# Optimization experiments

Measured on AMD Instinct MI355X. Metric: run time of the kernel, lower is better.

The kernel has to match this reference:

```python
import jax, jax.numpy as jnp
import numpy as np

N = 50000
E = 800000
IN_CH = 256
HEADS = 4
OUT_CH = 32
NEG_SLOPE = 0.2
EPS = 1e-16


def setup_inputs() -> dict:
    key = jax.random.key(0)
    k1, k2, k3, k4 = jax.random.split(key, 4)
    x = jax.random.normal(k1, (N, IN_CH), dtype=jnp.float32)
    edge_index = jax.random.randint(k2, (2, E), 0, N, dtype=jnp.int32)
    # xavier-ish scaling for stability
    weight = jax.random.normal(k3, (HEADS, IN_CH, OUT_CH), dtype=jnp.float32) * (1.0 / np.sqrt(IN_CH))
    att = jax.random.normal(k4, (HEADS, 2 * OUT_CH), dtype=jnp.float32) * (1.0 / np.sqrt(2 * OUT_CH))
    bias = jnp.zeros((HEADS * OUT_CH,), dtype=jnp.float32)
    return {"x": x, "edge_index": edge_index, "weight": weight, "att": att, "bias": bias}


def reference(x, edge_index, weight, att, bias):
    n = x.shape[0]
    H, C = weight.shape[0], weight.shape[2]
    src, dst = edge_index[0], edge_index[1]
    # node features -> per-head projected features [N,H,C]
    h = jnp.einsum('nf,hfc->nhc', x, weight)
    # per-node attention logits (equivalent to concat([h_src,h_dst]) . att)
    a_src = jnp.einsum('nhc,hc->nh', h, att[:, :C])  # [N,H]
    a_dst = jnp.einsum('nhc,hc->nh', h, att[:, C:])  # [N,H]
    alpha = a_src[src] + a_dst[dst]                  # [E,H]
    alpha = jnp.where(alpha > 0, alpha, NEG_SLOPE * alpha)  # LeakyReLU(0.2)
    # segment softmax over incoming edges of each dst node
    alpha_max = jnp.full((n, H), -1e9, dtype=alpha.dtype).at[dst].max(alpha)
    alpha_exp = jnp.exp(alpha - alpha_max[dst])
    sum_exp = jax.ops.segment_sum(alpha_exp, dst, num_segments=n)  # [N,H]
    a = alpha_exp / (sum_exp[dst] + EPS)             # [E,H]
    # weighted scatter-add aggregation
    msg = h[src] * a[:, :, None]                     # [E,H,C]
    out = jax.ops.segment_sum(msg, dst, num_segments=n)  # [N,H,C]
    out = out.reshape(n, H * C) + bias[None, :]
    return out
```

## Files before the change

### kernel.cpp

```cpp
#include <hip/hip_runtime.h>
#include <hip/hip_bf16.h>

#define NEG_SLOPE 0.2f
#define EPSF 1e-16f

typedef __attribute__((ext_vector_type(8))) short short8;
typedef __attribute__((ext_vector_type(4))) float floatx4;

__device__ __forceinline__ float bf2f(unsigned short u) {
  union { unsigned int i; float f; } v; v.i = ((unsigned int)u) << 16; return v.f;
}
__device__ __forceinline__ unsigned short f2bf(float f) {
  union { float f; unsigned int i; } v; v.f = f;
  unsigned int r = v.i + 0x7fffu + ((v.i >> 16) & 1u);
  return (unsigned short)(r >> 16);
}

__global__ __launch_bounds__(256) void prep_k(const unsigned short* __restrict__ xw,
                                              const void* __restrict__ w,
                                              const void* __restrict__ att,
                                              const void* __restrict__ bias,
                                              int* __restrict__ flag,
                                              int* __restrict__ cursor,
                                              int* __restrict__ ovf_cnt,
                                              unsigned short* __restrict__ bpack,
                                              unsigned short* __restrict__ wpack,
                                              float* __restrict__ bias_f,
                                              int n, int zb) {
  int b = blockIdx.x;
  if (b < zb) {
    int i = b * 256 + threadIdx.x;
    if (i < n) cursor[i] = 0;
    if (i == 0) *ovf_cnt = 0;
    return;
  }
  __shared__ int cnt;
  if (threadIdx.x == 0) cnt = 0;
  __syncthreads();
  int local = 0;
  for (int k2 = 0; k2 < 16; k2++) {
    unsigned short u = xw[(threadIdx.x * 16 + k2) << 1];
    int ex = (u >> 7) & 0xFF;
    if (ex >= 0x90 || ex <= 0x40) local++;
  }
  atomicAdd(&cnt, local);
  __syncthreads();
  int f32 = (cnt > 256) ? 1 : 0;
  int pb = b - zb;
  if (pb == 0 && threadIdx.x == 0) *flag = f32;
  if (pb < 128) {
    int i = pb * 256 + threadIdx.x;
    int j = i & 7, lane = (i >> 3) & 63, nt = (i >> 9) & 7, kb = i >> 12;
    int f = (kb << 5) + ((lane >> 4) << 3) + j;
    int col = (nt << 4) + (lane & 15);
    int src = ((col >> 5) << 13) + (f << 5) + (col & 31);
    float v = f32 ? ((const float*)w)[src] : bf2f(((const unsigned short*)w)[src]);
    bpack[i] = f2bf(v);
  } else if (pb < 144) {
    int i = (pb - 128) * 256 + threadIdx.x;
    int j = i & 7, lane = (i >> 3) & 63, kb = i >> 9;
    int quad = lane >> 4, m16 = lane & 15;
    int f = (kb << 5) + (quad << 3) + j;
    float v = 0.f;
    if (m16 < 8) {
      int hd = m16 & 3;
      int db = (m16 >= 4) ? 32 : 0;
      int wbase = (hd << 13) + (f << 5);
      int abase = (hd << 6) + db;
      float acc = 0.f;
      for (int c = 0; c < 32; c++) {
        float wv = f32 ? ((const float*)w)[wbase + c] : bf2f(((const unsigned short*)w)[wbase + c]);
        float av = f32 ? ((const float*)att)[abase + c] : bf2f(((const unsigned short*)att)[abase + c]);
        acc = fmaf(wv, av, acc);
      }
      v = acc;
    }
    wpack[i] = f2bf(v);
  } else {
    int i = threadIdx.x;
    if (i < 128) bias_f[i] = f32 ? ((const float*)bias)[i] : bf2f(((const unsigned short*)bias)[i]);
  }
}

__global__ __launch_bounds__(256) void gemmfill_k(const void* __restrict__ xv,
                                                  const int* __restrict__ flag,
                                                  const unsigned short* __restrict__ bpack,
                                                  const unsigned short* __restrict__ wpack,
                                                  unsigned short* __restrict__ h,
                                                  float* __restrict__ a_srcp,
                                                  float* __restrict__ a_dstp,
                                                  const int* __restrict__ ei,
                                                  int* __restrict__ cursor,
                                                  unsigned short* __restrict__ ed,
                                                  int2* __restrict__ ovf,
                                                  int* __restrict__ ovf_cnt,
                                                  int n, int e, int gb, int fb) {
  int b = blockIdx.x;
  if (b < gb) {
    int t = threadIdx.x;
    int wave = t >> 6, l = t & 63;
    int quad = l >> 4, m16 = l & 15;
    long n0 = (long)b * 128 + wave * 32;
    int isf32 = *flag;

    floatx4 acc[2][8];
    floatx4 acca[2];
#pragma unroll
    for (int mt = 0; mt < 2; mt++) {
      acca[mt] = (floatx4){0.f, 0.f, 0.f, 0.f};
#pragma unroll
      for (int nt = 0; nt < 8; nt++) acc[mt][nt] = (floatx4){0.f, 0.f, 0.f, 0.f};
    }

    for (int kb = 0; kb < 8; kb++) {
      short8 afr[2];
#pragma unroll
      for (int mt = 0; mt < 2; mt++) {
        long row = n0 + mt * 16 + m16;
        if (row >= n) row = n - 1;
        if (isf32) {
          const float* xp = (const float*)xv + (row << 8) + (kb << 5) + (quad << 3);
          float4 u0 = *(const float4*)xp;
          float4 u1 = *(const float4*)(xp + 4);
          short8 a;
          a[0] = (short)f2bf(u0.x); a[1] = (short)f2bf(u0.y);
          a[2] = (short)f2bf(u0.z); a[3] = (short)f2bf(u0.w);
          a[4] = (short)f2bf(u1.x); a[5] = (short)f2bf(u1.y);
          a[6] = (short)f2bf(u1.z); a[7] = (short)f2bf(u1.w);
          afr[mt] = a;
        } else {
          afr[mt] = *(const short8*)((const unsigned short*)xv + (row << 8) + (kb << 5) + (quad << 3));
        }
      }
      short8 wfr = *(const short8*)(wpack + (((kb << 6) + l) << 3));
      acca[0] = __builtin_amdgcn_mfma_f32_16x16x32_bf16(afr[0], wfr, acca[0], 0, 0, 0);
      acca[1] = __builtin_amdgcn_mfma_f32_16x16x32_bf16(afr[1], wfr, acca[1], 0, 0, 0);
#pragma unroll
      for (int nt = 0; nt < 8; nt++) {
        short8 bfr = *(const short8*)(bpack + (((kb << 3) + nt) << 9) + (l << 3));
        acc[0][nt] = __builtin_amdgcn_mfma_f32_16x16x32_bf16(afr[0], bfr, acc[0][nt], 0, 0, 0);
        acc[1][nt] = __builtin_amdgcn_mfma_f32_16x16x32_bf16(afr[1], bfr, acc[1][nt], 0, 0, 0);
      }
    }
#pragma unroll
    for (int mt = 0; mt < 2; mt++)
#pragma unroll
      for (int r = 0; r < 4; r++) {
        long row = n0 + mt * 16 + quad * 4 + r;
        if (row < n) {
#pragma unroll
          for (int nt = 0; nt < 8; nt++)
            h[(row << 7) + (nt << 4) + m16] = f2bf(acc[mt][nt][r]);
          if (m16 < 8) {
            float val = acca[mt][r];
            int hd = m16 & 3;
            if (m16 < 4) a_srcp[(row << 2) + hd] = val;
            else         a_dstp[(row << 2) + hd] = val;
          }
        }
      }
  } else {
    int fbi = b - gb;
    int k = b & 7;
    int shard = k >> 1;
    int sub = ((fbi >> 3) << 1) | (k & 1);
    int nsub = fb >> 2;
    int ns = (n + 3) >> 2;
    unsigned lo = (unsigned)(shard * ns);
    unsigned hi = (unsigned)min(n, (shard + 1) * ns);
    int nchunks = (e + 511) >> 9;
    for (int c = sub; c < nchunks; c += nsub) {
      int i0 = (c << 9) + threadIdx.x;
      int i1 = i0 + 256;
      unsigned d0 = 0xFFFFFFFFu, d1 = 0xFFFFFFFFu;
      int s0 = 0, s1 = 0;
      if (i0 < e) { d0 = (unsigned)ei[e + i0]; s0 = ei[i0]; }
      if (i1 < e) { d1 = (unsigned)ei[e + i1]; s1 = ei[i1]; }
      bool p0 = (d0 >= lo && d0 < hi);
      bool p1 = (d1 >= lo && d1 < hi);
      int c0 = -1, c1 = -1;
      if (p0) { if ((unsigned)s0 >= (unsigned)n) s0 = 0; c0 = atomicAdd(&cursor[d0], 1); }
      if (p1) { if ((unsigned)s1 >= (unsigned)n) s1 = 0; c1 = atomicAdd(&cursor[d1], 1); }
      if (p0) {
        if (c0 < 32) ed[((int)d0 << 5) + c0] = (unsigned short)s0;
        else { int kk = atomicAdd(ovf_cnt, 1); if (kk < e) ovf[kk] = make_int2((int)d0, s0); }
      }
      if (p1) {
        if (c1 < 32) ed[((int)d1 << 5) + c1] = (unsigned short)s1;
        else { int kk = atomicAdd(ovf_cnt, 1); if (kk < e) ovf[kk] = make_int2((int)d1, s1); }
      }
    }
  }
}

__global__ __launch_bounds__(512) void agg_k(const unsigned short* __restrict__ hfeat,
                                             const int* __restrict__ cursor,
                                             const unsigned short* __restrict__ ed,
                                             const int2* __restrict__ ovf,
                                             const int* __restrict__ ovf_cnt,
                                             const float* __restrict__ a_src,
                                             const float* __restrict__ a_dst,
                                             const float* __restrict__ bias_f,
                                             const int* __restrict__ flag,
                                             void* __restrict__ outv, int n, int e) {
  int wave = threadIdx.x >> 6;
  int l = threadIdx.x & 63;
  int node = (blockIdx.x << 3) + wave;
  if (node >= n) return;
  int total = cursor[node];
  int cnt0 = min(total, 32);
  int hq = l & 3;
  int c8 = l & 15;
  int hg = c8 >> 2;
  int q = l >> 4;
  float4 ad4 = *(const float4*)&a_dst[node << 2];
  float adq = (hq == 0) ? ad4.x : (hq == 1) ? ad4.y : (hq == 2) ? ad4.z : ad4.w;

  float m_run = -3.0e38f;
  float swacc = 0.f;
  float acc[8];
#pragma unroll
  for (int k = 0; k < 8; k++) acc[k] = 0.f;

  if (cnt0 > 0) {
    int srcv = 0;
    if (l < 32 && l < cnt0) srcv = (int)ed[(node << 5) + l];
    int myslot = l >> 2;
    int ssA = __shfl(srcv, myslot, 64);
    int ssB = __shfl(srcv, myslot + 16, 64);
    float zA = -3.0e38f, zB = -3.0e38f;
    if (myslot < cnt0) {
      float zz = a_src[(ssA << 2) + hq] + adq;
      zA = zz > 0.f ? zz : NEG_SLOPE * zz;
    }
    if (myslot + 16 < cnt0) {
      float zz = a_src[(ssB << 2) + hq] + adq;
      zB = zz > 0.f ? zz : NEG_SLOPE * zz;
    }
    float cm = fmaxf(zA, zB);
    cm = fmaxf(cm, __shfl_xor(cm, 4, 64));
    cm = fmaxf(cm, __shfl_xor(cm, 8, 64));
    cm = fmaxf(cm, __shfl_xor(cm, 16, 64));
    cm = fmaxf(cm, __shfl_xor(cm, 32, 64));
    float wexpA = (myslot < cnt0) ? __expf(zA - cm) : 0.f;
    float wexpB = (myslot + 16 < cnt0) ? __expf(zB - cm) : 0.f;
    m_run = cm;
    swacc = wexpA + wexpB;
    uint4 hv[8];
    int njs = (cnt0 + 3) >> 2;
#pragma unroll
    for (int j = 0; j < 8; j++) {
      if (j < njs) {
        int sj = __shfl(srcv, (j << 2) + q, 64);
        hv[j] = *(const uint4*)(hfeat + (((size_t)sj) << 7) + (c8 << 3));
      }
    }
#pragma unroll
    for (int j = 0; j < 8; j++) {
      if (j < njs) {
        int eidx = (j << 2) + q;
        float sw = (j < 4) ? __shfl(wexpA, (eidx << 2) | hg, 64)
                           : __shfl(wexpB, ((eidx - 16) << 2) | hg, 64);
        unsigned uu[4] = {hv[j].x, hv[j].y, hv[j].z, hv[j].w};
#pragma unroll
        for (int k2 = 0; k2 < 4; k2++) {
          acc[2 * k2]     = fmaf(sw, bf2f((unsigned short)(uu[k2] & 0xffffu)), acc[2 * k2]);
          acc[2 * k2 + 1] = fmaf(sw, bf2f((unsigned short)(uu[k2] >> 16)), acc[2 * k2 + 1]);
        }
      }
    }
  }

  if (total > 32) {
    int K = *ovf_cnt;
    if (K > e) K = e;
    for (int c0 = 0; c0 < K; c0 += 16) {
      int sv = 0, dv = -1;
      if (l < 16 && (c0 + l) < K) { int2 pr = ovf[c0 + l]; dv = pr.x; sv = pr.y; }
      int myslot = l >> 2;
      int dmy = __shfl(dv, myslot, 64);
      int smy = __shfl(sv, myslot, 64);
      bool valid = (dmy == node);
      float z = -3.0e38f;
      if (valid) {
        float zz = a_src[(smy << 2) + hq] + adq;
        z = zz > 0.f ? zz : NEG_SLOPE * zz;
      }
      float cm = z;
      cm = fmaxf(cm, __shfl_xor(cm, 4, 64));
      cm = fmaxf(cm, __shfl_xor(cm, 8, 64));
      cm = fmaxf(cm, __shfl_xor(cm, 16, 64));
      cm = fmaxf(cm, __shfl_xor(cm, 32, 64));
      float m_new = fmaxf(m_run, cm);
      float resc_q = __expf(m_run - m_new);
      m_run = m_new;
      float wexp = valid ? __expf(z - m_new) : 0.f;
      swacc = swacc * resc_q + wexp;
      float resc_h = __shfl(resc_q, hg, 64);
#pragma unroll
      for (int k = 0; k < 8; k++) acc[k] *= resc_h;
#pragma unroll
      for (int js = 0; js < 4; js++) {
        int eidx = (js << 2) + q;
        float sw = __shfl(wexp, (eidx << 2) | hg, 64);
        int sj = __shfl(sv, eidx, 64);
        uint4 hv = *(const uint4*)(hfeat + (((size_t)sj) << 7) + (c8 << 3));
        unsigned uu[4] = {hv.x, hv.y, hv.z, hv.w};
#pragma unroll
        for (int k2 = 0; k2 < 4; k2++) {
          acc[2 * k2]     = fmaf(sw, bf2f((unsigned short)(uu[k2] & 0xffffu)), acc[2 * k2]);
          acc[2 * k2 + 1] = fmaf(sw, bf2f((unsigned short)(uu[k2] >> 16)), acc[2 * k2 + 1]);
        }
      }
    }
  }

  for (int m = 4; m < 64; m <<= 1) swacc += __shfl_xor(swacc, m, 64);
#pragma unroll
  for (int k = 0; k < 8; k++) {
    acc[k] += __shfl_xor(acc[k], 16, 64);
    acc[k] += __shfl_xor(acc[k], 32, 64);
  }
  float sumv = __shfl(swacc, hg, 64);
  float rs = 1.f / (sumv + EPSF);
  if (l < 16) {
    float o[8];
#pragma unroll
    for (int k = 0; k < 8; k++) o[k] = fmaf(acc[k], rs, bias_f[(c8 << 3) + k]);
    size_t base = (((size_t)node) << 7) + (c8 << 3);
    if (*flag) {
      *(float4*)((float*)outv + base)     = make_float4(o[0], o[1], o[2], o[3]);
      *(float4*)((float*)outv + base + 4) = make_float4(o[4], o[5], o[6], o[7]);
    } else {
      uint4 pk;
      pk.x = (unsigned)f2bf(o[0]) | ((unsigned)f2bf(o[1]) << 16);
      pk.y = (unsigned)f2bf(o[2]) | ((unsigned)f2bf(o[3]) << 16);
      pk.z = (unsigned)f2bf(o[4]) | ((unsigned)f2bf(o[5]) << 16);
      pk.w = (unsigned)f2bf(o[6]) | ((unsigned)f2bf(o[7]) << 16);
      *(uint4*)((unsigned short*)outv + base) = pk;
    }
  }
}

extern "C" void kernel_launch(void* const* d_in, const int* in_sizes, int n_in,
                              void* d_out, int out_size, void* d_ws, size_t ws_size,
                              hipStream_t stream) {
  const void* x    = d_in[0];
  const int*  ei   = (const int*)d_in[1];
  const void* w    = d_in[2];
  const void* att  = d_in[3];
  const void* bias = d_in[4];

  const int n = in_sizes[0] / 256;
  const int e = in_sizes[1] / 2;
  const int zb = (n + 255) / 256;
  const int gb = (n + 127) / 128;
  const int fb = 2048;

  char* p = (char*)d_ws;
  size_t off = 0;
  auto carve = [&](size_t bytes) -> void* {
    void* r = p + off;
    off = (off + bytes + 255) & ~(size_t)255;
    return r;
  };
  int*      flag    = (int*)carve(sizeof(int));
  int*      ovf_cnt = (int*)carve(sizeof(int));
  float*    bias_f  = (float*)carve(128 * 4);
  unsigned short* h = (unsigned short*)carve((size_t)n * 128 * 2);
  float*    a_src   = (float*)carve((size_t)n * 4 * 4);
  float*    a_dst   = (float*)carve((size_t)n * 4 * 4);
  int*      cursor  = (int*)carve((size_t)n * 4);
  unsigned short* ed = (unsigned short*)carve((size_t)n * 32 * 2);
  int2*     ovf     = (int2*)carve((size_t)e * 8);
  unsigned short* bpack = (unsigned short*)carve((size_t)256 * 128 * 2);
  unsigned short* wpack = (unsigned short*)carve((size_t)8 * 64 * 8 * 2);
  (void)ws_size;

  prep_k<<<zb + 145, 256, 0, stream>>>((const unsigned short*)x, w, att, bias,
                                       flag, cursor, ovf_cnt, bpack, wpack, bias_f,
                                       n, zb);
  gemmfill_k<<<gb + fb, 256, 0, stream>>>(x, flag, bpack, wpack, h, a_src, a_dst,
                                          ei, cursor, ed, ovf, ovf_cnt, n, e, gb, fb);
  agg_k<<<(n + 7) / 8, 512, 0, stream>>>(h, cursor, ed, ovf, ovf_cnt, a_src, a_dst,
                                         bias_f, flag, d_out, n, e);
}
```

Measured before the change: 187.5 us.

## Unshard edge bucketing and hoist neighbor loads ahead of softmax in aggregation

The edge-fill branch previously had each of 2048 blocks stream the edge list and keep only destinations in one of four node shards, so every edge was read four times. It now launches one block per 512-edge chunk that handles all destinations directly, removing the redundant edge-index reads at the cost of more scattered atomics on cursor. In the aggregation kernel, the ed slot load, a_dst load, a_src gathers and all neighbor feature gathers are issued before the max/exp softmax math, so more memory latency can overlap. The extra in-flight loads raise register pressure.

```diff
diff --git a/kernel.cpp b/kernel.cpp
--- a/kernel.cpp
+++ b/kernel.cpp
@@ -160,35 +160,26 @@
         }
       }
   } else {
-    int fbi = b - gb;
-    int k = b & 7;
-    int shard = k >> 1;
-    int sub = ((fbi >> 3) << 1) | (k & 1);
-    int nsub = fb >> 2;
-    int ns = (n + 3) >> 2;
-    unsigned lo = (unsigned)(shard * ns);
-    unsigned hi = (unsigned)min(n, (shard + 1) * ns);
-    int nchunks = (e + 511) >> 9;
-    for (int c = sub; c < nchunks; c += nsub) {
-      int i0 = (c << 9) + threadIdx.x;
-      int i1 = i0 + 256;
-      unsigned d0 = 0xFFFFFFFFu, d1 = 0xFFFFFFFFu;
-      int s0 = 0, s1 = 0;
-      if (i0 < e) { d0 = (unsigned)ei[e + i0]; s0 = ei[i0]; }
-      if (i1 < e) { d1 = (unsigned)ei[e + i1]; s1 = ei[i1]; }
-      bool p0 = (d0 >= lo && d0 < hi);
-      bool p1 = (d1 >= lo && d1 < hi);
-      int c0 = -1, c1 = -1;
-      if (p0) { if ((unsigned)s0 >= (unsigned)n) s0 = 0; c0 = atomicAdd(&cursor[d0], 1); }
-      if (p1) { if ((unsigned)s1 >= (unsigned)n) s1 = 0; c1 = atomicAdd(&cursor[d1], 1); }
-      if (p0) {
-        if (c0 < 32) ed[((int)d0 << 5) + c0] = (unsigned short)s0;
-        else { int kk = atomicAdd(ovf_cnt, 1); if (kk < e) ovf[kk] = make_int2((int)d0, s0); }
-      }
-      if (p1) {
-        if (c1 < 32) ed[((int)d1 << 5) + c1] = (unsigned short)s1;
-        else { int kk = atomicAdd(ovf_cnt, 1); if (kk < e) ovf[kk] = make_int2((int)d1, s1); }
-      }
+    int c = b - gb;
+    int i0 = (c << 9) + threadIdx.x;
+    int i1 = i0 + 256;
+    unsigned d0 = 0, d1 = 0;
+    int s0 = 0, s1 = 0;
+    bool p0 = (i0 < e), p1 = (i1 < e);
+    if (p0) { d0 = (unsigned)ei[e + i0]; s0 = ei[i0]; }
+    if (p1) { d1 = (unsigned)ei[e + i1]; s1 = ei[i1]; }
+    if (p0 && d0 >= (unsigned)n) p0 = false;
+    if (p1 && d1 >= (unsigned)n) p1 = false;
+    int c0 = -1, c1 = -1;
+    if (p0) { if ((unsigned)s0 >= (unsigned)n) s0 = 0; c0 = atomicAdd(&cursor[d0], 1); }
+    if (p1) { if ((unsigned)s1 >= (unsigned)n) s1 = 0; c1 = atomicAdd(&cursor[d1], 1); }
+    if (p0) {
+      if (c0 < 32) ed[((int)d0 << 5) + c0] = (unsigned short)s0;
+      else { int kk = atomicAdd(ovf_cnt, 1); if (kk < e) ovf[kk] = make_int2((int)d0, s0); }
+    }
+    if (p1) {
+      if (c1 < 32) ed[((int)d1 << 5) + c1] = (unsigned short)s1;
+      else { int kk = atomicAdd(ovf_cnt, 1); if (kk < e) ovf[kk] = make_int2((int)d1, s1); }
     }
   }
 }
@@ -208,12 +199,14 @@
   int node = (blockIdx.x << 3) + wave;
   if (node >= n) return;
   int total = cursor[node];
+  int edv = (l < 32) ? (int)ed[(node << 5) + l] : 0;
+  float4 ad4 = *(const float4*)&a_dst[node << 2];
+
   int cnt0 = min(total, 32);
   int hq = l & 3;
   int c8 = l & 15;
   int hg = c8 >> 2;
   int q = l >> 4;
-  float4 ad4 = *(const float4*)&a_dst[node << 2];
   float adq = (hq == 0) ? ad4.x : (hq == 1) ? ad4.y : (hq == 2) ? ad4.z : ad4.w;
 
   float m_run = -3.0e38f;
@@ -223,18 +216,28 @@
   for (int k = 0; k < 8; k++) acc[k] = 0.f;
 
   if (cnt0 > 0) {
-    int srcv = 0;
-    if (l < 32 && l < cnt0) srcv = (int)ed[(node << 5) + l];
+    int srcv = (l < cnt0) ? edv : 0;
     int myslot = l >> 2;
     int ssA = __shfl(srcv, myslot, 64);
     int ssB = __shfl(srcv, myslot + 16, 64);
+    float asA = (myslot < cnt0) ? a_src[(ssA << 2) + hq] : 0.f;
+    float asB = (myslot + 16 < cnt0) ? a_src[(ssB << 2) + hq] : 0.f;
+    uint4 hv[8];
+    int njs = (cnt0 + 3) >> 2;
+#pragma unroll
+    for (int j = 0; j < 8; j++) {
+      if (j < njs) {
+        int sj = __shfl(srcv, (j << 2) + q, 64);
+        hv[j] = *(const uint4*)(hfeat + (((size_t)sj) << 7) + (c8 << 3));
+      }
+    }
     float zA = -3.0e38f, zB = -3.0e38f;
     if (myslot < cnt0) {
-      float zz = a_src[(ssA << 2) + hq] + adq;
+      float zz = asA + adq;
       zA = zz > 0.f ? zz : NEG_SLOPE * zz;
     }
     if (myslot + 16 < cnt0) {
-      float zz = a_src[(ssB << 2) + hq] + adq;
+      float zz = asB + adq;
       zB = zz > 0.f ? zz : NEG_SLOPE * zz;
     }
     float cm = fmaxf(zA, zB);
@@ -246,15 +249,6 @@
     float wexpB = (myslot + 16 < cnt0) ? __expf(zB - cm) : 0.f;
     m_run = cm;
     swacc = wexpA + wexpB;
-    uint4 hv[8];
-    int njs = (cnt0 + 3) >> 2;
-#pragma unroll
-    for (int j = 0; j < 8; j++) {
-      if (j < njs) {
-        int sj = __shfl(srcv, (j << 2) + q, 64);
-        hv[j] = *(const uint4*)(hfeat + (((size_t)sj) << 7) + (c8 << 3));
-      }
-    }
 #pragma unroll
     for (int j = 0; j < 8; j++) {
       if (j < njs) {
@@ -355,7 +349,7 @@
   const int e = in_sizes[1] / 2;
   const int zb = (n + 255) / 256;
   const int gb = (n + 127) / 128;
-  const int fb = 2048;
+  const int fb = (e + 511) / 512;
 
   char* p = (char*)d_ws;
   size_t off = 0;
```

After: 186.9 us. No clear change (-0.3%).
